# Kernel optimization log

Measured on AMD Instinct MI355X. Metric: run time of the kernel, lower is better.

Reference implementation:

```python
import jax, jax.numpy as jnp
import numpy as np
import math

N = 8192
DIM = 256

def setup_inputs() -> dict:
    key = jax.random.key(0)
    k1, k2, k3 = jax.random.split(key, 3)
    h = jax.random.normal(k1, (N, DIM), dtype=jnp.float32)
    # xavier_uniform with gain=1.414 for square [dim, dim] matrices
    gain = 1.414
    bound = gain * math.sqrt(6.0 / (DIM + DIM))
    Wq = jax.random.uniform(k2, (DIM, DIM), dtype=jnp.float32, minval=-bound, maxval=bound)
    Wk = jax.random.uniform(k3, (DIM, DIM), dtype=jnp.float32, minval=-bound, maxval=bound)
    return {"h": h, "Wq": Wq, "Wk": Wk}

def reference(h, Wq, Wk):
    dim = h.shape[1]
    q = h @ Wq                                   # [N, dim]
    k = h @ Wk                                   # [N, dim]
    e = (q @ k.T) / jnp.sqrt(jnp.asarray(dim, h.dtype))  # [N, N]
    attention = jax.nn.softmax(e, axis=1)        # row-wise softmax
    attention = attention.mean(axis=0)           # [N], column-mean over rows
    x = attention @ h                            # [dim]
    return x
```

## Files before the change

kernel.cpp:

```cpp
#include <hip/hip_runtime.h>
#include <cstdint>
#include <cstddef>


#define N_ROWS 8192
#define DIM    256

typedef __bf16 bf16x8 __attribute__((ext_vector_type(8)));
typedef unsigned short u16x8 __attribute__((ext_vector_type(8)));
typedef float f32x16 __attribute__((ext_vector_type(16)));

__device__ __forceinline__ uint16_t f2bf(float f) {
    uint32_t u = __float_as_uint(f);
    uint32_t r = (u + 0x7fffu + ((u >> 16) & 1u)) >> 16;
    return (uint16_t)r;
}

__device__ __forceinline__ float fexp2(float x) {
#if __has_builtin(__builtin_amdgcn_exp2f)
    return __builtin_amdgcn_exp2f(x);
#else
    return __expf(x * 0.69314718056f);
#endif
}

__device__ __forceinline__ void gld16(const void* gsrc, void* ldst) {
    __builtin_amdgcn_global_load_lds(
        (const __attribute__((address_space(1))) unsigned int*)gsrc,
        (__attribute__((address_space(3))) unsigned int*)ldst, 16, 0, 0);
}

__global__ __launch_bounds__(256) void proj_kernel(
        const float* __restrict__ h, const float* __restrict__ Wq,
        const float* __restrict__ Wk, uint16_t* __restrict__ qf,
        uint16_t* __restrict__ kf, float* __restrict__ l_arr,
        float* __restrict__ c_arr, float* __restrict__ out) {
    __shared__ alignas(16) float hbf[32 * 260];
    __shared__ alignas(16) uint16_t rep[4][1024];
    const int tid = threadIdx.x, lane = tid & 63, wave = tid >> 6;
    const int bid = blockIdx.x;
    const int rt = bid >> 2, ph = bid & 3;
    const int which = ph >> 1, p = ph & 1;

    if (bid < 32)       l_arr[bid * 256 + tid] = 0.0f;
    else if (bid < 64)  c_arr[(bid - 32) * 256 + tid] = 0.0f;
    else if (bid == 64) out[tid] = 0.0f;

    const float* __restrict__ W = which ? Wk : Wq;
    uint16_t* __restrict__ dst = which ? kf : qf;
    const float scale = which ? 1.0f : (0.0625f * 1.44269504089f);

    for (int i = tid; i < 2048; i += 256) {
        int r = i >> 6, c = (i & 63) * 4;
        *(float4*)&hbf[r * 260 + c] = *(const float4*)&h[(size_t)(rt * 32 + r) * DIM + c];
    }
    __syncthreads();

    bf16x8 afrag[16];
    {
        const int r = lane & 31;
#pragma unroll
        for (int a0 = 0; a0 < 16; a0++) {
            const int c0 = a0 * 16 + (lane >> 5) * 8;
            float4 f0 = *(const float4*)&hbf[r * 260 + c0];
            float4 f1 = *(const float4*)&hbf[r * 260 + c0 + 4];
            u16x8 f;
            f[0] = f2bf(f0.x); f[1] = f2bf(f0.y); f[2] = f2bf(f0.z); f[3] = f2bf(f0.w);
            f[4] = f2bf(f1.x); f[5] = f2bf(f1.y); f[6] = f2bf(f1.z); f[7] = f2bf(f1.w);
            afrag[a0] = __builtin_bit_cast(bf16x8, f);
        }
    }

    const int ctl = wave;
    const int cl = ctl * 32 + (lane & 31);
    f32x16 acc;
#pragma unroll
    for (int i = 0; i < 16; i++) acc[i] = 0.0f;
#pragma unroll
    for (int a0 = 0; a0 < 16; a0++) {
        const int kb = a0 * 16 + (lane >> 5) * 8;
        u16x8 f;
#pragma unroll
        for (int j = 0; j < 8; j++)
            f[j] = f2bf(W[(size_t)(kb + j) * DIM + p * 128 + cl]);
        acc = __builtin_amdgcn_mfma_f32_32x32x16_bf16(
            afrag[a0], __builtin_bit_cast(bf16x8, f), acc, 0, 0, 0);
    }

    {
        const int dcl = lane & 31;
        const int a0o = dcl >> 4, hi = (dcl >> 3) & 1, jj = dcl & 7;
        const int ilb = 4 * (lane >> 5);
#pragma unroll
        for (int reg = 0; reg < 16; reg++) {
            int il = ilb + (reg & 3) + 8 * (reg >> 2);
            rep[wave][(size_t)((a0o * 64) + il + 32 * hi) * 8 + jj] =
                f2bf(acc[reg] * scale);
        }
        const uint4* rv = (const uint4*)&rep[wave][0];
        uint4* gp = (uint4*)(dst + (size_t)rt * 8192 +
                             (size_t)(p * 4 + ctl) * 1024);
        gp[lane * 2]     = rv[lane * 2];
        gp[lane * 2 + 1] = rv[lane * 2 + 1];
    }
}

template <int MODE>
__global__ __launch_bounds__(512, 2) void qk_pass(
        const uint16_t* __restrict__ qf, const uint16_t* __restrict__ kf,
        float* __restrict__ l_arr, float* __restrict__ c_arr) {
    __shared__ alignas(16) uint16_t ktile[2][16384];
    __shared__ float c_lds[512];
    const int tid = threadIdx.x, lane = tid & 63, wave = tid >> 6;
    const int bid = blockIdx.x;
    const int cc = bid & 15, rb = bid >> 4;
    const int t0 = rb * 16 + wave * 2;
    const int row0 = t0 * 32;

    const uint4* qp = (const uint4*)qf;
    bf16x8 q0[16], q1[16];
#pragma unroll
    for (int a0 = 0; a0 < 16; a0++) {
        q0[a0] = __builtin_bit_cast(bf16x8, qp[(size_t)t0 * 1024 + a0 * 64 + lane]);
        q1[a0] = __builtin_bit_cast(bf16x8, qp[(size_t)(t0 + 1) * 1024 + a0 * 64 + lane]);
    }

    float rs0[16], rs1[16];
    float rr0[16], rr1[16];
    if (MODE == 0) {
#pragma unroll
        for (int r = 0; r < 16; r++) { rs0[r] = 0.0f; rs1[r] = 0.0f; }
    } else {
#pragma unroll
        for (int r = 0; r < 16; r++) {
            int ro = (r & 3) + 8 * (r >> 2) + 4 * (lane >> 5);
            rr0[r] = 1.0f / (8192.0f * l_arr[row0 + ro]);
            rr1[r] = 1.0f / (8192.0f * l_arr[row0 + 32 + ro]);
        }
        if (tid < 512) c_lds[tid] = 0.0f;
    }

    const char* ksrc = (const char*)kf + (size_t)cc * 16 * 16384;

    {
        const char* s0 = ksrc + wave * 4096 + lane * 16;
        char* d0 = (char*)&ktile[0][0] + wave * 4096;
#pragma unroll
        for (int it = 0; it < 4; it++) gld16(s0 + it * 1024, d0 + it * 1024);
    }

    for (int g = 0; g < 8; g++) {
        __syncthreads();
        if (g < 7) {
            const char* sn = ksrc + (size_t)(2 * g + 2) * 16384 + wave * 4096 + lane * 16;
            char* dn = (char*)&ktile[(g + 1) & 1][0] + wave * 4096;
#pragma unroll
            for (int it = 0; it < 4; it++) gld16(sn + it * 1024, dn + it * 1024);
        }

#pragma unroll
        for (int sub = 0; sub < 2; sub++) {
            const int t = 2 * g + sub;
            const uint16_t* kt = &ktile[g & 1][sub * 8192];
            f32x16 acc0, acc1;
#pragma unroll
            for (int i = 0; i < 16; i++) { acc0[i] = 0.0f; acc1[i] = 0.0f; }
#pragma unroll
            for (int a0 = 0; a0 < 16; a0++) {
                bf16x8 b = __builtin_bit_cast(bf16x8,
                    *(const u16x8*)&kt[(size_t)(a0 * 64 + lane) * 8]);
                acc0 = __builtin_amdgcn_mfma_f32_32x32x16_bf16(q0[a0], b, acc0, 0, 0, 0);
                acc1 = __builtin_amdgcn_mfma_f32_32x32x16_bf16(q1[a0], b, acc1, 0, 0, 0);
            }

            if (MODE == 0) {
#pragma unroll
                for (int r = 0; r < 16; r++) {
                    rs0[r] += fexp2(acc0[r]);
                    rs1[r] += fexp2(acc1[r]);
                }
            } else {
                float sv = 0.0f;
#pragma unroll
                for (int r = 0; r < 16; r++) {
                    sv += fexp2(acc0[r]) * rr0[r];
                    sv += fexp2(acc1[r]) * rr1[r];
                }
                sv += __shfl_xor(sv, 32);
                if (lane < 32) atomicAdd(&c_lds[t * 32 + lane], sv);
            }
        }
    }

    if (MODE == 0) {
#pragma unroll
        for (int r = 0; r < 16; r++) {
            float v0 = rs0[r], v1 = rs1[r];
            v0 += __shfl_xor(v0, 1);  v0 += __shfl_xor(v0, 2);
            v0 += __shfl_xor(v0, 4);  v0 += __shfl_xor(v0, 8);
            v0 += __shfl_xor(v0, 16);
            v1 += __shfl_xor(v1, 1);  v1 += __shfl_xor(v1, 2);
            v1 += __shfl_xor(v1, 4);  v1 += __shfl_xor(v1, 8);
            v1 += __shfl_xor(v1, 16);
            if ((lane & 31) == 0) {
                int ro = (r & 3) + 8 * (r >> 2) + 4 * (lane >> 5);
                atomicAdd(&l_arr[row0 + ro], v0);
                atomicAdd(&l_arr[row0 + 32 + ro], v1);
            }
        }
    } else {
        __syncthreads();
        if (tid < 512) atomicAdd(&c_arr[cc * 512 + tid], c_lds[tid]);
    }
}

__global__ __launch_bounds__(256) void finish_kernel(
        const float* __restrict__ h, const float* __restrict__ c_arr,
        float* __restrict__ out) {
    const int d = threadIdx.x;
    const int j0 = blockIdx.x * 32;
    float acc = 0.0f;
#pragma unroll
    for (int jj = 0; jj < 32; jj++)
        acc += c_arr[j0 + jj] * h[(size_t)(j0 + jj) * DIM + d];
    atomicAdd(&out[d], acc);
}

extern "C" void kernel_launch(void* const* d_in, const int* in_sizes, int n_in,
                              void* d_out, int out_size, void* d_ws, size_t ws_size,
                              hipStream_t stream) {
    const float* h  = (const float*)d_in[0];
    const float* Wq = (const float*)d_in[1];
    const float* Wk = (const float*)d_in[2];

    uint16_t* qf = (uint16_t*)d_ws;
    uint16_t* kf = qf + (size_t)N_ROWS * DIM;
    float* l_arr = (float*)((char*)d_ws + (size_t)8 * 1024 * 1024);
    float* c_arr = l_arr + N_ROWS;
    float* out = (float*)d_out;

    proj_kernel<<<1024, 256, 0, stream>>>(h, Wq, Wk, qf, kf, l_arr, c_arr, out);
    qk_pass<0><<<256, 512, 0, stream>>>(qf, kf, l_arr, c_arr);
    qk_pass<1><<<256, 512, 0, stream>>>(qf, kf, l_arr, c_arr);
    finish_kernel<<<256, 256, 0, stream>>>(h, c_arr, out);
}
```

Measured before the change: 147.4 us.

## Fuse both QK passes and finish into one cooperative kernel with grid syncs

```diff
diff --git a/kernel.cpp b/kernel.cpp
--- a/kernel.cpp
+++ b/kernel.cpp
@@ -1,10 +1,13 @@
 #include <hip/hip_runtime.h>
+#include <hip/hip_cooperative_groups.h>
 #include <cstdint>
 #include <cstddef>
 
 
 #define N_ROWS 8192
 #define DIM    256
+
+namespace cg = cooperative_groups;
 
 typedef __bf16 bf16x8 __attribute__((ext_vector_type(8)));
 typedef unsigned short u16x8 __attribute__((ext_vector_type(8)));
@@ -28,6 +31,10 @@
     __builtin_amdgcn_global_load_lds(
         (const __attribute__((address_space(1))) unsigned int*)gsrc,
         (__attribute__((address_space(3))) unsigned int*)ldst, 16, 0, 0);
+}
+
+__device__ __forceinline__ float agent_load(const float* p) {
+    return __hip_atomic_load(p, __ATOMIC_RELAXED, __HIP_MEMORY_SCOPE_AGENT);
 }
 
 __global__ __launch_bounds__(256) void proj_kernel(
@@ -105,12 +112,13 @@
     }
 }
 
-template <int MODE>
-__global__ __launch_bounds__(512, 2) void qk_pass(
+__global__ __launch_bounds__(512, 2) void qk_fused(
         const uint16_t* __restrict__ qf, const uint16_t* __restrict__ kf,
-        float* __restrict__ l_arr, float* __restrict__ c_arr) {
+        float* __restrict__ l_arr, float* __restrict__ c_arr,
+        const float* __restrict__ h, float* __restrict__ out) {
     __shared__ alignas(16) uint16_t ktile[2][16384];
     __shared__ float c_lds[512];
+    cg::grid_group grid = cg::this_grid();
     const int tid = threadIdx.x, lane = tid & 63, wave = tid >> 6;
     const int bid = blockIdx.x;
     const int cc = bid & 15, rb = bid >> 4;
@@ -125,74 +133,49 @@
         q1[a0] = __builtin_bit_cast(bf16x8, qp[(size_t)(t0 + 1) * 1024 + a0 * 64 + lane]);
     }
 
-    float rs0[16], rs1[16];
-    float rr0[16], rr1[16];
-    if (MODE == 0) {
+    const char* ksrc = (const char*)kf + (size_t)cc * 16 * 16384;
+
+    {
+        float rs0[16], rs1[16];
 #pragma unroll
         for (int r = 0; r < 16; r++) { rs0[r] = 0.0f; rs1[r] = 0.0f; }
-    } else {
-#pragma unroll
-        for (int r = 0; r < 16; r++) {
-            int ro = (r & 3) + 8 * (r >> 2) + 4 * (lane >> 5);
-            rr0[r] = 1.0f / (8192.0f * l_arr[row0 + ro]);
-            rr1[r] = 1.0f / (8192.0f * l_arr[row0 + 32 + ro]);
-        }
-        if (tid < 512) c_lds[tid] = 0.0f;
-    }
-
-    const char* ksrc = (const char*)kf + (size_t)cc * 16 * 16384;
-
-    {
-        const char* s0 = ksrc + wave * 4096 + lane * 16;
-        char* d0 = (char*)&ktile[0][0] + wave * 4096;
-#pragma unroll
-        for (int it = 0; it < 4; it++) gld16(s0 + it * 1024, d0 + it * 1024);
-    }
-
-    for (int g = 0; g < 8; g++) {
-        __syncthreads();
-        if (g < 7) {
-            const char* sn = ksrc + (size_t)(2 * g + 2) * 16384 + wave * 4096 + lane * 16;
-            char* dn = (char*)&ktile[(g + 1) & 1][0] + wave * 4096;
-#pragma unroll
-            for (int it = 0; it < 4; it++) gld16(sn + it * 1024, dn + it * 1024);
-        }
-
-#pragma unroll
-        for (int sub = 0; sub < 2; sub++) {
-            const int t = 2 * g + sub;
-            const uint16_t* kt = &ktile[g & 1][sub * 8192];
-            f32x16 acc0, acc1;
-#pragma unroll
-            for (int i = 0; i < 16; i++) { acc0[i] = 0.0f; acc1[i] = 0.0f; }
-#pragma unroll
-            for (int a0 = 0; a0 < 16; a0++) {
-                bf16x8 b = __builtin_bit_cast(bf16x8,
-                    *(const u16x8*)&kt[(size_t)(a0 * 64 + lane) * 8]);
-                acc0 = __builtin_amdgcn_mfma_f32_32x32x16_bf16(q0[a0], b, acc0, 0, 0, 0);
-                acc1 = __builtin_amdgcn_mfma_f32_32x32x16_bf16(q1[a0], b, acc1, 0, 0, 0);
-            }
-
-            if (MODE == 0) {
+
+        {
+            const char* s0 = ksrc + wave * 4096 + lane * 16;
+            char* d0 = (char*)&ktile[0][0] + wave * 4096;
+#pragma unroll
+            for (int it = 0; it < 4; it++) gld16(s0 + it * 1024, d0 + it * 1024);
+        }
+
+        for (int g = 0; g < 8; g++) {
+            __syncthreads();
+            if (g < 7) {
+                const char* sn = ksrc + (size_t)(2 * g + 2) * 16384 + wave * 4096 + lane * 16;
+                char* dn = (char*)&ktile[(g + 1) & 1][0] + wave * 4096;
+#pragma unroll
+                for (int it = 0; it < 4; it++) gld16(sn + it * 1024, dn + it * 1024);
+            }
+#pragma unroll
+            for (int sub = 0; sub < 2; sub++) {
+                const uint16_t* kt = &ktile[g & 1][sub * 8192];
+                f32x16 acc0, acc1;
+#pragma unroll
+                for (int i = 0; i < 16; i++) { acc0[i] = 0.0f; acc1[i] = 0.0f; }
+#pragma unroll
+                for (int a0 = 0; a0 < 16; a0++) {
+                    bf16x8 b = __builtin_bit_cast(bf16x8,
+                        *(const u16x8*)&kt[(size_t)(a0 * 64 + lane) * 8]);
+                    acc0 = __builtin_amdgcn_mfma_f32_32x32x16_bf16(q0[a0], b, acc0, 0, 0, 0);
+                    acc1 = __builtin_amdgcn_mfma_f32_32x32x16_bf16(q1[a0], b, acc1, 0, 0, 0);
+                }
 #pragma unroll
                 for (int r = 0; r < 16; r++) {
                     rs0[r] += fexp2(acc0[r]);
                     rs1[r] += fexp2(acc1[r]);
                 }
-            } else {
-                float sv = 0.0f;
-#pragma unroll
-                for (int r = 0; r < 16; r++) {
-                    sv += fexp2(acc0[r]) * rr0[r];
-                    sv += fexp2(acc1[r]) * rr1[r];
-                }
-                sv += __shfl_xor(sv, 32);
-                if (lane < 32) atomicAdd(&c_lds[t * 32 + lane], sv);
-            }
-        }
-    }
-
-    if (MODE == 0) {
+            }
+        }
+
 #pragma unroll
         for (int r = 0; r < 16; r++) {
             float v0 = rs0[r], v1 = rs1[r];
@@ -208,22 +191,77 @@
                 atomicAdd(&l_arr[row0 + 32 + ro], v1);
             }
         }
-    } else {
+    }
+
+    __threadfence();
+    grid.sync();
+
+    {
+        float rr0[16], rr1[16];
+#pragma unroll
+        for (int r = 0; r < 16; r++) {
+            int ro = (r & 3) + 8 * (r >> 2) + 4 * (lane >> 5);
+            rr0[r] = 1.0f / (8192.0f * agent_load(&l_arr[row0 + ro]));
+            rr1[r] = 1.0f / (8192.0f * agent_load(&l_arr[row0 + 32 + ro]));
+        }
+        if (tid < 512) c_lds[tid] = 0.0f;
+
+        {
+            const char* s0 = ksrc + wave * 4096 + lane * 16;
+            char* d0 = (char*)&ktile[0][0] + wave * 4096;
+#pragma unroll
+            for (int it = 0; it < 4; it++) gld16(s0 + it * 1024, d0 + it * 1024);
+        }
+
+        for (int g = 0; g < 8; g++) {
+            __syncthreads();
+            if (g < 7) {
+                const char* sn = ksrc + (size_t)(2 * g + 2) * 16384 + wave * 4096 + lane * 16;
+                char* dn = (char*)&ktile[(g + 1) & 1][0] + wave * 4096;
+#pragma unroll
+                for (int it = 0; it < 4; it++) gld16(sn + it * 1024, dn + it * 1024);
+            }
+#pragma unroll
+            for (int sub = 0; sub < 2; sub++) {
+                const int t = 2 * g + sub;
+                const uint16_t* kt = &ktile[g & 1][sub * 8192];
+                f32x16 acc0, acc1;
+#pragma unroll
+                for (int i = 0; i < 16; i++) { acc0[i] = 0.0f; acc1[i] = 0.0f; }
+#pragma unroll
+                for (int a0 = 0; a0 < 16; a0++) {
+                    bf16x8 b = __builtin_bit_cast(bf16x8,
+                        *(const u16x8*)&kt[(size_t)(a0 * 64 + lane) * 8]);
+                    acc0 = __builtin_amdgcn_mfma_f32_32x32x16_bf16(q0[a0], b, acc0, 0, 0, 0);
+                    acc1 = __builtin_amdgcn_mfma_f32_32x32x16_bf16(q1[a0], b, acc1, 0, 0, 0);
+                }
+                float sv = 0.0f;
+#pragma unroll
+                for (int r = 0; r < 16; r++) {
+                    sv += fexp2(acc0[r]) * rr0[r];
+                    sv += fexp2(acc1[r]) * rr1[r];
+                }
+                sv += __shfl_xor(sv, 32);
+                if (lane < 32) atomicAdd(&c_lds[t * 32 + lane], sv);
+            }
+        }
+
         __syncthreads();
         if (tid < 512) atomicAdd(&c_arr[cc * 512 + tid], c_lds[tid]);
     }
-}
-
-__global__ __launch_bounds__(256) void finish_kernel(
-        const float* __restrict__ h, const float* __restrict__ c_arr,
-        float* __restrict__ out) {
-    const int d = threadIdx.x;
-    const int j0 = blockIdx.x * 32;
-    float acc = 0.0f;
-#pragma unroll
-    for (int jj = 0; jj < 32; jj++)
-        acc += c_arr[j0 + jj] * h[(size_t)(j0 + jj) * DIM + d];
-    atomicAdd(&out[d], acc);
+
+    __threadfence();
+    grid.sync();
+
+    if (tid < 256) {
+        const int d = tid;
+        const int j0 = bid * 32;
+        float acc = 0.0f;
+#pragma unroll
+        for (int jj = 0; jj < 32; jj++)
+            acc += agent_load(&c_arr[j0 + jj]) * h[(size_t)(j0 + jj) * DIM + d];
+        atomicAdd(&out[d], acc);
+    }
 }
 
 extern "C" void kernel_launch(void* const* d_in, const int* in_sizes, int n_in,
@@ -240,7 +278,9 @@
     float* out = (float*)d_out;
 
     proj_kernel<<<1024, 256, 0, stream>>>(h, Wq, Wk, qf, kf, l_arr, c_arr, out);
-    qk_pass<0><<<256, 512, 0, stream>>>(qf, kf, l_arr, c_arr);
-    qk_pass<1><<<256, 512, 0, stream>>>(qf, kf, l_arr, c_arr);
-    finish_kernel<<<256, 256, 0, stream>>>(h, c_arr, out);
-}
+
+    void* kargs[] = {(void*)&qf, (void*)&kf, (void*)&l_arr, (void*)&c_arr,
+                     (void*)&h, (void*)&out};
+    hipLaunchCooperativeKernel(reinterpret_cast<void*>(&qk_fused),
+                               dim3(256), dim3(512), kargs, 0, stream);
+}
```

Result: slower. 281.8 us (+91.1%).
